# Kernel tuning notes

Measured on AMD Instinct MI355X. Metric: run time of the kernel, lower is better.

The kernel has to match this reference:

```python
import jax, jax.numpy as jnp
import numpy as np

N, E, F, DE, G, C = 50000, 800000, 64, 32, 512, 2
EPS = 1e-5


def setup_inputs() -> dict:
    key = jax.random.key(0)
    ks = jax.random.split(key, 12)
    Z = 2 * F + DE  # CGConv concat dim [x_i, x_j, edge_attr]
    inp = {
        "x": jax.random.normal(ks[0], (N, F), dtype=jnp.float32),
        "edge_index": jax.random.randint(ks[1], (2, E), 0, N, dtype=jnp.int32),
        "edge_attr": jax.random.normal(ks[2], (E, DE), dtype=jnp.float32),
        "batch": jnp.sort(jax.random.randint(ks[3], (N,), 0, G, dtype=jnp.int32)),
        # CGConv lin_f / lin_s : (2F+De) -> F, with bias
        "Wf": jax.random.normal(ks[4], (Z, F), dtype=jnp.float32) * 0.05,
        "bf": jnp.zeros((F,), dtype=jnp.float32),
        "Ws": jax.random.normal(ks[5], (Z, F), dtype=jnp.float32) * 0.05,
        "bs": jnp.zeros((F,), dtype=jnp.float32),
        # CGConv internal BatchNorm (training-mode batch stats)
        "bn_w": jnp.ones((F,), dtype=jnp.float32),
        "bn_b": jnp.zeros((F,), dtype=jnp.float32),
        # PyG LayerNorm (graph mode, batch=None -> whole-tensor stats)
        "ln_w": jnp.ones((F,), dtype=jnp.float32),
        "ln_b": jnp.zeros((F,), dtype=jnp.float32),
        # final linear (2F -> C) and output LayerNorm
        "Wl": jax.random.normal(ks[6], (2 * F, C), dtype=jnp.float32) * 0.05,
        "bl": jnp.zeros((C,), dtype=jnp.float32),
        "ln4_w": jnp.ones((C,), dtype=jnp.float32),
        "ln4_b": jnp.zeros((C,), dtype=jnp.float32),
    }
    return inp


def _pyg_layernorm(x, w, b):
    # torch_geometric.nn.LayerNorm, mode='graph', batch=None: whole-tensor stats
    xc = x - jnp.mean(x)
    out = xc / (jnp.sqrt(jnp.mean(xc * xc)) + EPS)
    return out * w + b


def reference(x, edge_index, edge_attr, batch, Wf, bf, Ws, bs, bn_w, bn_b,
              ln_w, ln_b, Wl, bl, ln4_w, ln4_b):
    src = edge_index[0]  # x_j (source)
    dst = edge_index[1]  # x_i (target / aggregation index)

    # CGConv message: sigmoid(lin_f(z)) * softplus(lin_s(z)), z=[x_i,x_j,e]
    z = jnp.concatenate([x[dst], x[src], edge_attr], axis=1)  # [E, 2F+De]
    msg = jax.nn.sigmoid(z @ Wf + bf) * jax.nn.softplus(z @ Ws + bs)  # [E,F]

    # scatter-add aggregation to target nodes
    agg = jax.ops.segment_sum(msg, dst, num_segments=N)  # [N,F]

    # CGConv batch_norm=True (training-mode batch statistics over nodes)
    mu = jnp.mean(agg, axis=0)
    var = jnp.mean((agg - mu) ** 2, axis=0)
    agg = (agg - mu) / jnp.sqrt(var + EPS) * bn_w + bn_b

    # residual
    h = agg + x

    # LayerNorm + softplus
    h = jax.nn.softplus(_pyg_layernorm(h, ln_w, ln_b))

    # global mean / add pooling over graphs
    add_pool = jax.ops.segment_sum(h, batch, num_segments=G)  # [G,F]
    counts = jax.ops.segment_sum(jnp.ones((N,), h.dtype), batch, num_segments=G)
    mean_pool = add_pool / jnp.maximum(counts, 1.0)[:, None]

    g = jnp.concatenate([mean_pool, add_pool], axis=1)  # [G, 2F]
    out = g @ Wl + bl  # [G, C]
    out = _pyg_layernorm(out, ln4_w, ln4_b)
    return out
```

## Files before the change

kernel.cpp:

```cpp
#include <hip/hip_runtime.h>
#include <math.h>

#define EPSF 1e-5f

typedef short bf16x8 __attribute__((ext_vector_type(8)));
typedef float f32x4 __attribute__((ext_vector_type(4)));

static __device__ __forceinline__ unsigned short f2bf(float x) {
  unsigned u = __float_as_uint(x);
  unsigned r = (u + 0x7FFFu + ((u >> 16) & 1u)) >> 16;
  return (unsigned short)r;
}

static __device__ __forceinline__ float msgv(float F, float S) {
  float sig = __builtin_amdgcn_rcpf(1.0f + __expf(-F));
  float sp = fmaxf(S, 0.f) + __logf(1.0f + __expf(-fabsf(S)));
  return sig * sp;
}

static __device__ __forceinline__ void gload16(const void* g, void* l) {
  __builtin_amdgcn_global_load_lds(
      (const __attribute__((address_space(1))) unsigned int*)g,
      (__attribute__((address_space(3))) unsigned int*)l, 16, 0, 0);
}

__global__ __launch_bounds__(256) void prep_kernel(
    const float* __restrict__ x, const float* __restrict__ Wf,
    const float* __restrict__ Ws, const int* __restrict__ ei,
    unsigned short* __restrict__ xbf, unsigned short* __restrict__ Bfrag,
    int* __restrict__ deg, int NCV, int total8, int E) {
  const int b = blockIdx.x, t = threadIdx.x;
  if (b < NCV) {
    int i = b * 256 + t;
    if (i < total8) {
      float4 a = ((const float4*)x)[i * 2];
      float4 c = ((const float4*)x)[i * 2 + 1];
      unsigned short o[8];
      o[0] = f2bf(a.x); o[1] = f2bf(a.y); o[2] = f2bf(a.z); o[3] = f2bf(a.w);
      o[4] = f2bf(c.x); o[5] = f2bf(c.y); o[6] = f2bf(c.z); o[7] = f2bf(c.w);
      ((uint4*)xbf)[i] = *(uint4*)o;
    }
  } else if (b < NCV + 10) {
    int g2 = (b - NCV) * 256 + t;
    if (g2 < 2560) {
      const int ks = g2 >> 9, t8 = (g2 >> 6) & 7, l = g2 & 63;
      const int q = l & 15, g = l >> 4;
      const float* W = (t8 < 4) ? Wf : Ws;
      const int col = (t8 & 3) * 16 + q;
      unsigned short out[8];
#pragma unroll
      for (int i = 0; i < 8; ++i) {
        int kk = ks * 32 + g * 8 + i;
        int wr = (kk < 32) ? (128 + kk) : (kk - 32);
        out[i] = f2bf(W[(size_t)wr * 64 + col]);
      }
      *(uint4*)&Bfrag[((size_t)(ks * 8 + t8) * 64 + l) * 8] = *(uint4*)out;
    }
  } else {
    int i = (b - NCV - 10) * 256 + t;
    if (i < E) atomicAdd(&deg[ei[E + i]], 1);
  }
}

__global__ __launch_bounds__(256) void scan_a(const int* __restrict__ deg,
                                              int* __restrict__ bsum, int N) {
  const int idx = blockIdx.x * 256 + threadIdx.x;
  int v = (idx < N) ? deg[idx] : 0;
#pragma unroll
  for (int o = 32; o > 0; o >>= 1) v += __shfl_down(v, o);
  __shared__ int ws4[4];
  if ((threadIdx.x & 63) == 0) ws4[threadIdx.x >> 6] = v;
  __syncthreads();
  if (threadIdx.x == 0) bsum[blockIdx.x] = ws4[0] + ws4[1] + ws4[2] + ws4[3];
}

__global__ __launch_bounds__(256) void scan_b(const int* __restrict__ bsum,
                                              int* __restrict__ bpre, int NB) {
  const int t = threadIdx.x;
  const int lane = t & 63, w = t >> 6;
  int v = (t < NB) ? bsum[t] : 0;
  int sc = v;
#pragma unroll
  for (int o = 1; o < 64; o <<= 1) {
    int u = __shfl_up(sc, o);
    if (lane >= o) sc += u;
  }
  __shared__ int wsum[4];
  if (lane == 63) wsum[w] = sc;
  __syncthreads();
  int add = 0;
#pragma unroll
  for (int k = 0; k < 4; ++k) add += (k < w) ? wsum[k] : 0;
  bpre[t] = (sc - v) + add;
}

__global__ __launch_bounds__(256) void scan_c(const int* __restrict__ deg,
                                              const int* __restrict__ bpre,
                                              int* __restrict__ cursor, int N) {
  const int t = threadIdx.x;
  const int lane = t & 63, w = t >> 6;
  const int idx = blockIdx.x * 256 + t;
  int d = (idx < N) ? deg[idx] : 0;
  int sc = d;
#pragma unroll
  for (int o = 1; o < 64; o <<= 1) {
    int u = __shfl_up(sc, o);
    if (lane >= o) sc += u;
  }
  __shared__ int wsum[4];
  if (lane == 63) wsum[w] = sc;
  __syncthreads();
  int add = bpre[blockIdx.x];
#pragma unroll
  for (int k = 0; k < 4; ++k) add += (k < w) ? wsum[k] : 0;
  if (idx < N) cursor[idx] = add + (sc - d);
}

__global__ void scatter_kernel(const int* __restrict__ ei,
                               int* __restrict__ cursor,
                               int2* __restrict__ epk, int E) {
  int i = blockIdx.x * 256 + threadIdx.x;
  if (i >= E) return;
  int dst = ei[E + i];
  int pos = atomicAdd(&cursor[dst], 1);
  epk[pos] = make_int2(i, (ei[i] & 0xFFFF) | (dst << 16));
}

__global__ __launch_bounds__(256) void edge_fused(
    const int2* __restrict__ epk, const float* __restrict__ eattr,
    const unsigned short* __restrict__ xbf,
    const unsigned short* __restrict__ Bfrag, const float* __restrict__ bf_,
    const float* __restrict__ bs_, float* __restrict__ agg, int T16, int N,
    int E) {
  __shared__ __align__(16) unsigned char Bls[40960];
  __shared__ __align__(16) unsigned char AshA[40960];

  for (int i = threadIdx.x; i < 2560; i += 256)
    ((uint4*)Bls)[i] = ((const uint4*)Bfrag)[i];
  __syncthreads();

  const int lane = threadIdx.x & 63, w = threadIdx.x >> 6;
  const int q = lane & 15, g = lane >> 4;
  const int row = lane >> 2, c = lane & 3;
  const int cs = c ^ ((row >> 1) & 3);

  const int nB = gridDim.x;
  const int cb = (blockIdx.x & 7) * (nB >> 3) + (blockIdx.x >> 3);
  const int qT = T16 / nB, rT = T16 - qT * nB;
  const int bt0 = cb * qT + min(cb, rT);
  const int bt1 = bt0 + qT + (cb < rT ? 1 : 0);
  const int blen = bt1 - bt0;
  const int per = (blen + 3) >> 2;
  const int wt0 = bt0 + w * per;
  const int wt1 = min(bt1, wt0 + per);
  if (wt0 >= wt1) return;
  const int tlast = wt1 - 1;

  float bfv[4], bsv[4];
#pragma unroll
  for (int cg = 0; cg < 4; ++cg) {
    bfv[cg] = bf_[cg * 16 + q];
    bsv[cg] = bs_[cg * 16 + q];
  }

  char* myA = (char*)AshA + w * 10240;

  auto STAGE_LOADS = [&](int bufSel, int2 er, float4& e0, float4& e1) {
    unsigned eid = ((unsigned)er.x < (unsigned)E) ? (unsigned)er.x : 0u;
    unsigned sv = (unsigned)er.y;
    unsigned su = sv & 0xFFFFu;
    if (su >= (unsigned)N) su = 0;
    unsigned du = sv >> 16;
    if (du >= (unsigned)N) du = 0;
    char* base = myA + bufSel * 5120;
    gload16(xbf + (size_t)du * 64 + cs * 8, base + 1024);
    gload16(xbf + (size_t)du * 64 + 32 + cs * 8, base + 2048);
    gload16(xbf + (size_t)su * 64 + cs * 8, base + 3072);
    gload16(xbf + (size_t)su * 64 + 32 + cs * 8, base + 4096);
    const float* ep_ = eattr + (size_t)eid * 32 + cs * 8;
    e0 = *(const float4*)ep_;
    e1 = *(const float4*)(ep_ + 4);
  };
  auto EATTR_WRITE = [&](int bufSel, float4 e0, float4 e1) {
    bf16x8 sv;
    sv[0] = (short)f2bf(e0.x); sv[1] = (short)f2bf(e0.y);
    sv[2] = (short)f2bf(e0.z); sv[3] = (short)f2bf(e0.w);
    sv[4] = (short)f2bf(e1.x); sv[5] = (short)f2bf(e1.y);
    sv[6] = (short)f2bf(e1.z); sv[7] = (short)f2bf(e1.w);
    *(bf16x8*)(myA + bufSel * 5120 + row * 64 + c * 16) = sv;
  };

  int tcur = wt0;
  int2 eprow = epk[(size_t)tcur * 16 + row];
  int2 epq = epk[(size_t)tcur * 16 + q];
  float4 a0, a1;
  STAGE_LOADS(0, eprow, a0, a1);
  const int t1i = min(tcur + 1, tlast);
  int2 eprow_n = epk[(size_t)t1i * 16 + row];
  int2 epq_n = epk[(size_t)t1i * 16 + q];
  EATTR_WRITE(0, a0, a1);
  int buf = 0;

  for (;;) {
    const int t2i = min(tcur + 2, tlast);
    float4 b0, b1;
    STAGE_LOADS(buf ^ 1, eprow_n, b0, b1);
    int2 eprow_nn = epk[(size_t)t2i * 16 + row];
    int2 epq_nn = epk[(size_t)t2i * 16 + q];
    __builtin_amdgcn_sched_barrier(0);
    asm volatile("s_waitcnt vmcnt(8)" ::: "memory");
    asm volatile("s_waitcnt lgkmcnt(0)" ::: "memory");
    __builtin_amdgcn_sched_barrier(0);

    const char* Ab = myA + buf * 5120;
    f32x4 accf[4], accs[4];
#pragma unroll
    for (int nt = 0; nt < 4; ++nt) {
      accf[nt] = (f32x4){0.f, 0.f, 0.f, 0.f};
      accs[nt] = (f32x4){0.f, 0.f, 0.f, 0.f};
    }
#pragma unroll
    for (int ks = 0; ks < 5; ++ks) {
      const bf16x8 a =
          *(const bf16x8*)(Ab + ks * 1024 + q * 64 + ((g ^ ((q >> 1) & 3)) << 4));
#pragma unroll
      for (int nt = 0; nt < 4; ++nt) {
        const bf16x8 Bfr =
            *(const bf16x8*)(Bls + (((ks * 8 + nt) * 64 + lane) << 4));
        const bf16x8 Bsr =
            *(const bf16x8*)(Bls + (((ks * 8 + 4 + nt) * 64 + lane) << 4));
        accf[nt] =
            __builtin_amdgcn_mfma_f32_16x16x32_bf16(a, Bfr, accf[nt], 0, 0, 0);
        accs[nt] =
            __builtin_amdgcn_mfma_f32_16x16x32_bf16(a, Bsr, accs[nt], 0, 0, 0);
      }
    }

    EATTR_WRITE(buf ^ 1, b0, b1);

    const unsigned dA = ((unsigned)__shfl(epq.y, 0)) >> 16;
    const unsigned dB = ((unsigned)__shfl(epq.y, 15)) >> 16;
    if (dA == dB) {
      float tot0, tot1, tot2, tot3;
#pragma unroll
      for (int cg = 0; cg < 4; ++cg) {
        float s = msgv(accf[cg][0] + bfv[cg], accs[cg][0] + bsv[cg]) +
                  msgv(accf[cg][1] + bfv[cg], accs[cg][1] + bsv[cg]) +
                  msgv(accf[cg][2] + bfv[cg], accs[cg][2] + bsv[cg]) +
                  msgv(accf[cg][3] + bfv[cg], accs[cg][3] + bsv[cg]);
        s += __shfl_xor(s, 16);
        s += __shfl_xor(s, 32);
        if (cg == 0) tot0 = s;
        else if (cg == 1) tot1 = s;
        else if (cg == 2) tot2 = s;
        else tot3 = s;
      }
      float v = (g == 0) ? tot0 : (g == 1) ? tot1 : (g == 2) ? tot2 : tot3;
      if (dA < (unsigned)N) atomicAdd(&agg[(size_t)dA * 64 + g * 16 + q], v);
    } else {
      const unsigned d0 = ((unsigned)__shfl(epq.y, g * 4)) >> 16;
      const unsigned d1 = ((unsigned)__shfl(epq.y, g * 4 + 1)) >> 16;
      const unsigned d2 = ((unsigned)__shfl(epq.y, g * 4 + 2)) >> 16;
      const unsigned d3 = ((unsigned)__shfl(epq.y, g * 4 + 3)) >> 16;
#pragma unroll
      for (int cg = 0; cg < 4; ++cg) {
        const int feat = cg * 16 + q;
        unsigned dc = d0;
        float a_ = msgv(accf[cg][0] + bfv[cg], accs[cg][0] + bsv[cg]);
#define STEP(DR, RIDX)                                                        \
  {                                                                           \
    unsigned dr = (DR);                                                       \
    if (dr != dc) {                                                           \
      if (dc < (unsigned)N) atomicAdd(&agg[(size_t)dc * 64 + feat], a_);      \
      dc = dr;                                                                \
      a_ = 0.f;                                                               \
    }                                                                         \
    a_ += msgv(accf[cg][RIDX] + bfv[cg], accs[cg][RIDX] + bsv[cg]);           \
  }
        STEP(d1, 1)
        STEP(d2, 2)
        STEP(d3, 3)
#undef STEP
        if (dc < (unsigned)N) atomicAdd(&agg[(size_t)dc * 64 + feat], a_);
      }
    }

    if (tcur == tlast) break;
    tcur += 1;
    eprow_n = eprow_nn;
    epq = epq_n;
    epq_n = epq_nn;
    buf ^= 1;
  }
}

__global__ __launch_bounds__(256) void stats_kernel(
    const float* __restrict__ agg, const float* __restrict__ x,
    float* __restrict__ stats, int N) {
  const int f = threadIdx.x & 63;
  const int sub = threadIdx.x >> 6;
  float sa = 0, sa2 = 0, sx = 0, sx2 = 0, sax = 0;
  for (int r = blockIdx.x * 4 + sub; r < N; r += gridDim.x * 4) {
    float a = agg[(size_t)r * 64 + f];
    float xv = x[(size_t)r * 64 + f];
    sa += a; sa2 += a * a; sx += xv; sx2 += xv * xv; sax += a * xv;
  }
  __shared__ float lds[4][5][64];
  lds[sub][0][f] = sa; lds[sub][1][f] = sa2; lds[sub][2][f] = sx;
  lds[sub][3][f] = sx2; lds[sub][4][f] = sax;
  __syncthreads();
  if (sub == 0) {
#pragma unroll
    for (int i = 0; i < 5; ++i) {
      float v = lds[0][i][f] + lds[1][i][f] + lds[2][i][f] + lds[3][i][f];
      atomicAdd(&stats[i * 64 + f], v);
    }
  }
}

__global__ __launch_bounds__(256) void node_finish(
    const float* __restrict__ stats, const float* __restrict__ bn_w,
    const float* __restrict__ bn_b, const float* __restrict__ agg,
    const float* __restrict__ x, const int* __restrict__ batch,
    const float* __restrict__ ln_w, const float* __restrict__ ln_b,
    float* __restrict__ add_pool, float* __restrict__ counts, int N,
    int chunk) {
  const int f = threadIdx.x & 63;
  const int sub = threadIdx.x >> 6;
  const float Nf = (float)N;
  const float invN = 1.0f / Nf;
  float Sa = stats[f], Sa2 = stats[64 + f], Sx = stats[128 + f],
        Sx2 = stats[192 + f], Sax = stats[256 + f];
  float mu = Sa * invN;
  float var = Sa2 * invN - mu * mu;
  const float alpha = bn_w[f] / sqrtf(var + EPSF);
  const float beta = bn_b[f] - mu * alpha;
  float Sh = alpha * Sa + Nf * beta + Sx;
  float Sh2 = alpha * alpha * Sa2 + Sx2 + Nf * beta * beta +
              2.f * alpha * Sax + 2.f * alpha * beta * Sa + 2.f * beta * Sx;
#pragma unroll
  for (int o = 32; o > 0; o >>= 1) {
    Sh += __shfl_xor(Sh, o);
    Sh2 += __shfl_xor(Sh2, o);
  }
  const float cnt = Nf * 64.0f;
  const float mean = Sh / cnt;
  const float msq = Sh2 / cnt - mean * mean;
  const float rden = 1.0f / (sqrtf(fmaxf(msq, 0.f)) + EPSF);
  const float lw = ln_w[f] * rden;
  const float lb = ln_b[f];

  const int r0 = blockIdx.x * chunk;
  const int r1 = min(N, r0 + chunk);
  float acc = 0.f, cacc = 0.f;
  int curg = -1;
  for (int r = r0 + sub; r < r1; r += 4) {
    int g = batch[r];
    if (g != curg) {
      if (curg >= 0) {
        atomicAdd(&add_pool[(size_t)curg * 64 + f], acc);
        if (f == 0) atomicAdd(&counts[curg], cacc);
      }
      curg = g; acc = 0.f; cacc = 0.f;
    }
    float h = fmaf(alpha, agg[(size_t)r * 64 + f], beta) + x[(size_t)r * 64 + f];
    float v = (h - mean) * lw + lb;
    float sp = fmaxf(v, 0.f) + __logf(1.0f + __expf(-fabsf(v)));
    acc += sp; cacc += 1.f;
  }
  if (curg >= 0) {
    atomicAdd(&add_pool[(size_t)curg * 64 + f], acc);
    if (f == 0) atomicAdd(&counts[curg], cacc);
  }
}

__global__ __launch_bounds__(1024) void graph_out(
    const float* __restrict__ add_pool, const float* __restrict__ counts,
    const float* __restrict__ Wl, const float* __restrict__ bl,
    const float* __restrict__ w4, const float* __restrict__ b4,
    float* __restrict__ out, int G) {
  const int t = threadIdx.x;
  const int g = t >> 1, c = t & 1;
  float cnt = fmaxf(counts[g], 1.0f);
  float inv = 1.0f / cnt;
  const float4* ap4 = (const float4*)(add_pool + (size_t)g * 64);
  const float4* W4 = (const float4*)Wl;
  float v = bl[c];
#pragma unroll 4
  for (int k4 = 0; k4 < 16; ++k4) {
    float4 a4 = ap4[k4];
    float4 wa = W4[k4 * 2];
    float4 wb = W4[k4 * 2 + 1];
    float4 wc = W4[32 + k4 * 2];
    float4 wd = W4[32 + k4 * 2 + 1];
    float m0 = c ? wa.y : wa.x, m1 = c ? wa.w : wa.z;
    float m2 = c ? wb.y : wb.x, m3 = c ? wb.w : wb.z;
    float a0 = c ? wc.y : wc.x, a1 = c ? wc.w : wc.z;
    float a2 = c ? wd.y : wd.x, a3 = c ? wd.w : wd.z;
    v = fmaf(a4.x, fmaf(m0, inv, a0), v);
    v = fmaf(a4.y, fmaf(m1, inv, a1), v);
    v = fmaf(a4.z, fmaf(m2, inv, a2), v);
    v = fmaf(a4.w, fmaf(m3, inv, a3), v);
  }

  __shared__ float red[16];
  __shared__ float bc[2];
  float sum = v;
#pragma unroll
  for (int o = 32; o > 0; o >>= 1) sum += __shfl_down(sum, o);
  if ((t & 63) == 0) red[t >> 6] = sum;
  __syncthreads();
  if (t == 0) {
    float tot = 0;
#pragma unroll
    for (int i = 0; i < 16; ++i) tot += red[i];
    bc[0] = tot * (1.0f / 1024.0f);
  }
  __syncthreads();
  const float mean = bc[0];
  const float xc = v - mean;
  float sq = xc * xc;
  __syncthreads();
#pragma unroll
  for (int o = 32; o > 0; o >>= 1) sq += __shfl_down(sq, o);
  if ((t & 63) == 0) red[t >> 6] = sq;
  __syncthreads();
  if (t == 0) {
    float tot = 0;
#pragma unroll
    for (int i = 0; i < 16; ++i) tot += red[i];
    bc[1] = 1.0f / (sqrtf(tot * (1.0f / 1024.0f)) + EPSF);
  }
  __syncthreads();
  out[t] = xc * bc[1] * w4[c] + b4[c];
}

extern "C" void kernel_launch(void* const* d_in, const int* in_sizes, int n_in,
                              void* d_out, int out_size, void* d_ws,
                              size_t ws_size, hipStream_t stream) {
  const float* x = (const float*)d_in[0];
  const int* ei = (const int*)d_in[1];
  const float* eattr = (const float*)d_in[2];
  const int* batch = (const int*)d_in[3];
  const float* Wf = (const float*)d_in[4];
  const float* bf = (const float*)d_in[5];
  const float* Ws = (const float*)d_in[6];
  const float* bs = (const float*)d_in[7];
  const float* bn_w = (const float*)d_in[8];
  const float* bn_b = (const float*)d_in[9];
  const float* ln_w = (const float*)d_in[10];
  const float* ln_b = (const float*)d_in[11];
  const float* Wl = (const float*)d_in[12];
  const float* bl = (const float*)d_in[13];
  const float* w4 = (const float*)d_in[14];
  const float* b4 = (const float*)d_in[15];

  const int N = in_sizes[0] / 64;
  const int E = in_sizes[2] / 32;
  const int G = 512;
  const int NB = (N + 255) / 256;
  const int T16 = (E + 15) / 16;
  const int NCV = (N * 8 + 255) / 256;
  const int NH = (E + 255) / 256;

  float* ws = (float*)d_ws;
  float* agg = ws;
  float* stats = agg + (size_t)N * 64;
  float* add_pool = stats + 320;
  float* counts = add_pool + (size_t)G * 64;
  int* deg = (int*)(counts + G);
  int* cursor = deg + N;
  int* bsum = cursor + N;
  int* bpre = bsum + 256;
  unsigned short* Bfrag = (unsigned short*)(bpre + 256);
  unsigned short* xbf = Bfrag + 20480;
  int2* epk = (int2*)(xbf + (size_t)N * 64);

  size_t zeroFloats = (size_t)N * 64 + 320 + (size_t)G * 64 + G + N;
  hipMemsetAsync(agg, 0, zeroFloats * sizeof(float), stream);
  const int padE = T16 * 16 - E;
  if (padE > 0) hipMemsetAsync(epk + E, 0xFF, (size_t)padE * 8, stream);

  prep_kernel<<<NCV + 10 + NH, 256, 0, stream>>>(x, Wf, Ws, ei, xbf, Bfrag,
                                                 deg, NCV, N * 8, E);
  scan_a<<<NB, 256, 0, stream>>>(deg, bsum, N);
  scan_b<<<1, 256, 0, stream>>>(bsum, bpre, NB);
  scan_c<<<NB, 256, 0, stream>>>(deg, bpre, cursor, N);
  scatter_kernel<<<NH, 256, 0, stream>>>(ei, cursor, epk, E);
  edge_fused<<<512, 256, 0, stream>>>(epk, eattr, xbf, Bfrag, bf, bs, agg, T16,
                                      N, E);
  stats_kernel<<<512, 256, 0, stream>>>(agg, x, stats, N);
  const int chunk = (N + 511) / 512;
  node_finish<<<512, 256, 0, stream>>>(stats, bn_w, bn_b, agg, x, batch, ln_w,
                                       ln_b, add_pool, counts, N, chunk);
  graph_out<<<1, 1024, 0, stream>>>(add_pool, counts, Wl, bl, w4, b4,
                                    (float*)d_out, G);
}
```

Before: 303.5 us.

## Pad CSR into per-destination 16-edge tiles and pre-pack bf16 edge attributes

```diff
diff --git a/kernel.cpp b/kernel.cpp
--- a/kernel.cpp
+++ b/kernel.cpp
@@ -65,7 +65,7 @@
 __global__ __launch_bounds__(256) void scan_a(const int* __restrict__ deg,
                                               int* __restrict__ bsum, int N) {
   const int idx = blockIdx.x * 256 + threadIdx.x;
-  int v = (idx < N) ? deg[idx] : 0;
+  int v = (idx < N) ? ((deg[idx] + 15) >> 4) : 0;
 #pragma unroll
   for (int o = 32; o > 0; o >>= 1) v += __shfl_down(v, o);
   __shared__ int ws4[4];
@@ -75,7 +75,9 @@
 }
 
 __global__ __launch_bounds__(256) void scan_b(const int* __restrict__ bsum,
-                                              int* __restrict__ bpre, int NB) {
+                                              int* __restrict__ bpre,
+                                              int* __restrict__ tile_total,
+                                              int NB) {
   const int t = threadIdx.x;
   const int lane = t & 63, w = t >> 6;
   int v = (t < NB) ? bsum[t] : 0;
@@ -92,15 +94,17 @@
 #pragma unroll
   for (int k = 0; k < 4; ++k) add += (k < w) ? wsum[k] : 0;
   bpre[t] = (sc - v) + add;
+  if (t == 255) tile_total[0] = sc + add;
 }
 
 __global__ __launch_bounds__(256) void scan_c(const int* __restrict__ deg,
                                               const int* __restrict__ bpre,
-                                              int* __restrict__ cursor, int N) {
+                                              int* __restrict__ cursor,
+                                              int* __restrict__ tstart, int N) {
   const int t = threadIdx.x;
   const int lane = t & 63, w = t >> 6;
   const int idx = blockIdx.x * 256 + t;
-  int d = (idx < N) ? deg[idx] : 0;
+  int d = (idx < N) ? ((deg[idx] + 15) >> 4) : 0;
   int sc = d;
 #pragma unroll
   for (int o = 1; o < 64; o <<= 1) {
@@ -113,25 +117,50 @@
   int add = bpre[blockIdx.x];
 #pragma unroll
   for (int k = 0; k < 4; ++k) add += (k < w) ? wsum[k] : 0;
-  if (idx < N) cursor[idx] = add + (sc - d);
-}
-
-__global__ void scatter_kernel(const int* __restrict__ ei,
-                               int* __restrict__ cursor,
-                               int2* __restrict__ epk, int E) {
+  if (idx < N) {
+    int ts = add + (sc - d);
+    tstart[idx] = ts;
+    cursor[idx] = ts * 16;
+  }
+}
+
+__global__ __launch_bounds__(256) void scatter_pack(
+    const int* __restrict__ ei, int* __restrict__ cursor,
+    const int* __restrict__ deg, const int* __restrict__ tstart,
+    const float* __restrict__ eattr, int* __restrict__ epk,
+    int* __restrict__ thdr, unsigned short* __restrict__ eabf, int E) {
   int i = blockIdx.x * 256 + threadIdx.x;
   if (i >= E) return;
-  int dst = ei[E + i];
-  int pos = atomicAdd(&cursor[dst], 1);
-  epk[pos] = make_int2(i, (ei[i] & 0xFFFF) | (dst << 16));
+  const int src = ei[i];
+  const int dst = ei[E + i];
+  const int pos = atomicAdd(&cursor[dst], 1);
+  epk[pos] = (src & 0xFFFF) | (dst << 16);
+  const int ts = tstart[dst];
+  const int k = pos - ts * 16;
+  if ((k & 15) == 0) {
+    int vc = min(16, deg[dst] - (k & ~15));
+    thdr[ts + (k >> 4)] = dst | (vc << 16);
+  }
+  const float4* er = (const float4*)(eattr + (size_t)i * 32);
+  unsigned short o[32];
+#pragma unroll
+  for (int kk = 0; kk < 8; ++kk) {
+    float4 v = er[kk];
+    o[kk * 4] = f2bf(v.x); o[kk * 4 + 1] = f2bf(v.y);
+    o[kk * 4 + 2] = f2bf(v.z); o[kk * 4 + 3] = f2bf(v.w);
+  }
+  uint4* dp = (uint4*)(eabf + (size_t)pos * 32);
+#pragma unroll
+  for (int kk = 0; kk < 4; ++kk) dp[kk] = ((uint4*)o)[kk];
 }
 
 __global__ __launch_bounds__(256) void edge_fused(
-    const int2* __restrict__ epk, const float* __restrict__ eattr,
+    const int* __restrict__ epk, const int* __restrict__ thdr,
+    const unsigned short* __restrict__ eabf,
     const unsigned short* __restrict__ xbf,
     const unsigned short* __restrict__ Bfrag, const float* __restrict__ bf_,
-    const float* __restrict__ bs_, float* __restrict__ agg, int T16, int N,
-    int E) {
+    const float* __restrict__ bs_, float* __restrict__ agg,
+    const int* __restrict__ tile_total, int N) {
   __shared__ __align__(16) unsigned char Bls[40960];
   __shared__ __align__(16) unsigned char AshA[40960];
 
@@ -144,9 +173,10 @@
   const int row = lane >> 2, c = lane & 3;
   const int cs = c ^ ((row >> 1) & 3);
 
+  const int T = tile_total[0];
   const int nB = gridDim.x;
   const int cb = (blockIdx.x & 7) * (nB >> 3) + (blockIdx.x >> 3);
-  const int qT = T16 / nB, rT = T16 - qT * nB;
+  const int qT = T / nB, rT = T - qT * nB;
   const int bt0 = cb * qT + min(cb, rT);
   const int bt1 = bt0 + qT + (cb < rT ? 1 : 0);
   const int blen = bt1 - bt0;
@@ -165,51 +195,37 @@
 
   char* myA = (char*)AshA + w * 10240;
 
-  auto STAGE_LOADS = [&](int bufSel, int2 er, float4& e0, float4& e1) {
-    unsigned eid = ((unsigned)er.x < (unsigned)E) ? (unsigned)er.x : 0u;
-    unsigned sv = (unsigned)er.y;
-    unsigned su = sv & 0xFFFFu;
+  auto STAGE = [&](int bufSel, int tile, int er) {
+    unsigned su = (unsigned)(er & 0xFFFF);
     if (su >= (unsigned)N) su = 0;
-    unsigned du = sv >> 16;
+    unsigned du = ((unsigned)er) >> 16;
     if (du >= (unsigned)N) du = 0;
     char* base = myA + bufSel * 5120;
+    gload16(eabf + ((size_t)tile * 16 + row) * 32 + cs * 8, base);
     gload16(xbf + (size_t)du * 64 + cs * 8, base + 1024);
     gload16(xbf + (size_t)du * 64 + 32 + cs * 8, base + 2048);
     gload16(xbf + (size_t)su * 64 + cs * 8, base + 3072);
     gload16(xbf + (size_t)su * 64 + 32 + cs * 8, base + 4096);
-    const float* ep_ = eattr + (size_t)eid * 32 + cs * 8;
-    e0 = *(const float4*)ep_;
-    e1 = *(const float4*)(ep_ + 4);
   };
-  auto EATTR_WRITE = [&](int bufSel, float4 e0, float4 e1) {
-    bf16x8 sv;
-    sv[0] = (short)f2bf(e0.x); sv[1] = (short)f2bf(e0.y);
-    sv[2] = (short)f2bf(e0.z); sv[3] = (short)f2bf(e0.w);
-    sv[4] = (short)f2bf(e1.x); sv[5] = (short)f2bf(e1.y);
-    sv[6] = (short)f2bf(e1.z); sv[7] = (short)f2bf(e1.w);
-    *(bf16x8*)(myA + bufSel * 5120 + row * 64 + c * 16) = sv;
-  };
-
+
+  atomicAdd(&agg[lane], 0.0f);
   int tcur = wt0;
-  int2 eprow = epk[(size_t)tcur * 16 + row];
-  int2 epq = epk[(size_t)tcur * 16 + q];
-  float4 a0, a1;
-  STAGE_LOADS(0, eprow, a0, a1);
+  int ep_c = epk[(size_t)tcur * 16 + row];
+  int hdr_cur = thdr[tcur];
+  STAGE(0, tcur, ep_c);
   const int t1i = min(tcur + 1, tlast);
-  int2 eprow_n = epk[(size_t)t1i * 16 + row];
-  int2 epq_n = epk[(size_t)t1i * 16 + q];
-  EATTR_WRITE(0, a0, a1);
+  int ep_next = epk[(size_t)t1i * 16 + row];
+  int hdr_next = thdr[t1i];
   int buf = 0;
 
   for (;;) {
+    const int tn = min(tcur + 1, tlast);
     const int t2i = min(tcur + 2, tlast);
-    float4 b0, b1;
-    STAGE_LOADS(buf ^ 1, eprow_n, b0, b1);
-    int2 eprow_nn = epk[(size_t)t2i * 16 + row];
-    int2 epq_nn = epk[(size_t)t2i * 16 + q];
+    STAGE(buf ^ 1, tn, ep_next);
+    int ep_nn = epk[(size_t)t2i * 16 + row];
+    int hdr_nn = thdr[t2i];
     __builtin_amdgcn_sched_barrier(0);
     asm volatile("s_waitcnt vmcnt(8)" ::: "memory");
-    asm volatile("s_waitcnt lgkmcnt(0)" ::: "memory");
     __builtin_amdgcn_sched_barrier(0);
 
     const char* Ab = myA + buf * 5120;
@@ -236,61 +252,36 @@
       }
     }
 
-    EATTR_WRITE(buf ^ 1, b0, b1);
-
-    const unsigned dA = ((unsigned)__shfl(epq.y, 0)) >> 16;
-    const unsigned dB = ((unsigned)__shfl(epq.y, 15)) >> 16;
-    if (dA == dB) {
-      float tot0, tot1, tot2, tot3;
-#pragma unroll
-      for (int cg = 0; cg < 4; ++cg) {
-        float s = msgv(accf[cg][0] + bfv[cg], accs[cg][0] + bsv[cg]) +
-                  msgv(accf[cg][1] + bfv[cg], accs[cg][1] + bsv[cg]) +
-                  msgv(accf[cg][2] + bfv[cg], accs[cg][2] + bsv[cg]) +
-                  msgv(accf[cg][3] + bfv[cg], accs[cg][3] + bsv[cg]);
-        s += __shfl_xor(s, 16);
-        s += __shfl_xor(s, 32);
-        if (cg == 0) tot0 = s;
-        else if (cg == 1) tot1 = s;
-        else if (cg == 2) tot2 = s;
-        else tot3 = s;
+    const int dstT = hdr_cur & 0xFFFF;
+    const int vcnt = hdr_cur >> 16;
+    float tot0, tot1, tot2, tot3;
+#pragma unroll
+    for (int cg = 0; cg < 4; ++cg) {
+      float s = 0.f;
+#pragma unroll
+      for (int r = 0; r < 4; ++r) {
+        float m = msgv(accf[cg][r] + bfv[cg], accs[cg][r] + bsv[cg]);
+        s += (g * 4 + r < vcnt) ? m : 0.f;
       }
-      float v = (g == 0) ? tot0 : (g == 1) ? tot1 : (g == 2) ? tot2 : tot3;
-      if (dA < (unsigned)N) atomicAdd(&agg[(size_t)dA * 64 + g * 16 + q], v);
-    } else {
-      const unsigned d0 = ((unsigned)__shfl(epq.y, g * 4)) >> 16;
-      const unsigned d1 = ((unsigned)__shfl(epq.y, g * 4 + 1)) >> 16;
-      const unsigned d2 = ((unsigned)__shfl(epq.y, g * 4 + 2)) >> 16;
-      const unsigned d3 = ((unsigned)__shfl(epq.y, g * 4 + 3)) >> 16;
-#pragma unroll
-      for (int cg = 0; cg < 4; ++cg) {
-        const int feat = cg * 16 + q;
-        unsigned dc = d0;
-        float a_ = msgv(accf[cg][0] + bfv[cg], accs[cg][0] + bsv[cg]);
-#define STEP(DR, RIDX)                                                        \
-  {                                                                           \
-    unsigned dr = (DR);                                                       \
-    if (dr != dc) {                                                           \
-      if (dc < (unsigned)N) atomicAdd(&agg[(size_t)dc * 64 + feat], a_);      \
-      dc = dr;                                                                \
-      a_ = 0.f;                                                               \
-    }                                                                         \
-    a_ += msgv(accf[cg][RIDX] + bfv[cg], accs[cg][RIDX] + bsv[cg]);           \
-  }
-        STEP(d1, 1)
-        STEP(d2, 2)
-        STEP(d3, 3)
-#undef STEP
-        if (dc < (unsigned)N) atomicAdd(&agg[(size_t)dc * 64 + feat], a_);
-      }
-    }
+      s += __shfl_xor(s, 16);
+      s += __shfl_xor(s, 32);
+      if (cg == 0) tot0 = s;
+      else if (cg == 1) tot1 = s;
+      else if (cg == 2) tot2 = s;
+      else tot3 = s;
+    }
+    float v = (g == 0) ? tot0 : (g == 1) ? tot1 : (g == 2) ? tot2 : tot3;
+    unsigned dd = (unsigned)dstT;
+    float vv = (dd < (unsigned)N) ? v : 0.f;
+    dd = min(dd, (unsigned)(N - 1));
+    atomicAdd(&agg[(size_t)dd * 64 + g * 16 + q], vv);
 
     if (tcur == tlast) break;
     tcur += 1;
-    eprow_n = eprow_nn;
-    epq = epq_n;
-    epq_n = epq_nn;
     buf ^= 1;
+    hdr_cur = hdr_next;
+    hdr_next = hdr_nn;
+    ep_next = ep_nn;
   }
 }
 
@@ -459,9 +450,9 @@
   const int E = in_sizes[2] / 32;
   const int G = 512;
   const int NB = (N + 255) / 256;
-  const int T16 = (E + 15) / 16;
   const int NCV = (N * 8 + 255) / 256;
   const int NH = (E + 255) / 256;
+  const int Tcap = N + (E + 15) / 16;
 
   float* ws = (float*)d_ws;
   float* agg = ws;
@@ -470,25 +461,29 @@
   float* counts = add_pool + (size_t)G * 64;
   int* deg = (int*)(counts + G);
   int* cursor = deg + N;
-  int* bsum = cursor + N;
+  int* tstart = cursor + N;
+  int* tile_total = tstart + N;
+  int* bsum = tile_total + 4;
   int* bpre = bsum + 256;
   unsigned short* Bfrag = (unsigned short*)(bpre + 256);
   unsigned short* xbf = Bfrag + 20480;
-  int2* epk = (int2*)(xbf + (size_t)N * 64);
+  int* thdr = (int*)(xbf + (size_t)N * 64);
+  int* epk = thdr + Tcap;
+  unsigned short* eabf = (unsigned short*)(epk + (size_t)Tcap * 16);
 
   size_t zeroFloats = (size_t)N * 64 + 320 + (size_t)G * 64 + G + N;
   hipMemsetAsync(agg, 0, zeroFloats * sizeof(float), stream);
-  const int padE = T16 * 16 - E;
-  if (padE > 0) hipMemsetAsync(epk + E, 0xFF, (size_t)padE * 8, stream);
+  hipMemsetAsync(epk, 0, (size_t)Tcap * 16 * sizeof(int), stream);
 
   prep_kernel<<<NCV + 10 + NH, 256, 0, stream>>>(x, Wf, Ws, ei, xbf, Bfrag,
                                                  deg, NCV, N * 8, E);
   scan_a<<<NB, 256, 0, stream>>>(deg, bsum, N);
-  scan_b<<<1, 256, 0, stream>>>(bsum, bpre, NB);
-  scan_c<<<NB, 256, 0, stream>>>(deg, bpre, cursor, N);
-  scatter_kernel<<<NH, 256, 0, stream>>>(ei, cursor, epk, E);
-  edge_fused<<<512, 256, 0, stream>>>(epk, eattr, xbf, Bfrag, bf, bs, agg, T16,
-                                      N, E);
+  scan_b<<<1, 256, 0, stream>>>(bsum, bpre, tile_total, NB);
+  scan_c<<<NB, 256, 0, stream>>>(deg, bpre, cursor, tstart, N);
+  scatter_pack<<<NH, 256, 0, stream>>>(ei, cursor, deg, tstart, eattr, epk,
+                                       thdr, eabf, E);
+  edge_fused<<<512, 256, 0, stream>>>(epk, thdr, eabf, xbf, Bfrag, bf, bs, agg,
+                                      tile_total, N);
   stats_kernel<<<512, 256, 0, stream>>>(agg, x, stats, N);
   const int chunk = (N + 511) / 512;
   node_finish<<<512, 256, 0, stream>>>(stats, bn_w, bn_b, agg, x, batch, ln_w,
```

Result: slower. 323.1 us (+6.4%).
